# Kernel tuning notes

Measured on AMD Instinct MI355X. Metric: run time of the kernel, lower is better.

Reference implementation:

```python
import jax, jax.numpy as jnp
import numpy as np

EPS = 1e-6

def rms_norm(x):
    # RMSNorm over last dim, no learned weight (torch F.rms_norm without weight)
    return x * jax.lax.rsqrt(jnp.mean(jnp.square(x), axis=-1, keepdims=True) + EPS)

def apply_rotary_emb(x, cos, sin):
    # x: [b, t, h, d]; cos/sin: [t, d//2] -> broadcast [1, t, 1, d//2]
    half = x.shape[-1] // 2
    c = cos[None, :, None, :]
    s = sin[None, :, None, :]
    x1, x2 = x[..., :half], x[..., half:]
    return jnp.concatenate([x1 * c - x2 * s, x2 * c + x1 * s], axis=-1)

def setup_inputs() -> dict:
    key = jax.random.key(0)
    ks = jax.random.split(key, 16)
    B, T, E, H = 4, 2048, 1024, 16
    D = E // H
    inp = {
        "query": jax.random.normal(ks[0], (B, T, E), jnp.float32),
        "key": jax.random.normal(ks[1], (B, T, E), jnp.float32),
        "value": jax.random.normal(ks[2], (B, T, E), jnp.float32),
        "attn_mask": jnp.tril(jnp.ones((T, T), dtype=bool)),
        "cos": jnp.cos(jnp.arange(T)[:, None] / (10000.0 ** (jnp.arange(D // 2) / (D // 2)))[None, :]).astype(jnp.float32),
        "sin": jnp.sin(jnp.arange(T)[:, None] / (10000.0 ** (jnp.arange(D // 2) / (D // 2)))[None, :]).astype(jnp.float32),
        "Wq": jax.random.normal(ks[3], (E, E), jnp.float32) * 0.02,
        "bq": jnp.zeros((E,), jnp.float32),
        "Wk": jax.random.normal(ks[4], (E, E), jnp.float32) * 0.02,
        "bk": jnp.zeros((E,), jnp.float32),
        "Wv": jax.random.normal(ks[5], (E, E), jnp.float32) * 0.02,
        "bv": jnp.zeros((E,), jnp.float32),
        "Wo": jax.random.normal(ks[6], (E, E), jnp.float32) * 0.02,
        "bo": jnp.zeros((E,), jnp.float32),
    }
    return inp

def reference(query, key, value, attn_mask, cos, sin, Wq, bq, Wk, bk, Wv, bv, Wo, bo):
    B, T, E = query.shape
    H = 16
    D = E // H
    q = query @ Wq.T + bq
    k = key @ Wk.T + bk
    v = value @ Wv.T + bv
    q = q.reshape(B, T, H, D)
    k = k.reshape(B, T, H, D)
    v = v.reshape(B, T, H, D)
    q, k = rms_norm(q), rms_norm(k)
    q = apply_rotary_emb(q, cos, sin)
    k = apply_rotary_emb(k, cos, sin)
    # SDPA: [b, h, t, d] layout via einsum directly from [b, t, h, d]
    scale = 1.0 / jnp.sqrt(jnp.float32(D))
    scores = jnp.einsum('bqhd,bkhd->bhqk', q, k) * scale
    scores = jnp.where(attn_mask[None, None, :, :], scores, jnp.float32(-jnp.inf))
    attn = jax.nn.softmax(scores, axis=-1)
    o = jnp.einsum('bhqk,bkhd->bqhd', attn, v).reshape(B, T, E)
    return o @ Wo.T + bo
```

## Files before the change

kernel.cpp:

```cpp
#include <hip/hip_runtime.h>

typedef __bf16 bf16;
typedef __bf16 bf16x8 __attribute__((ext_vector_type(8)));
typedef __bf16 bf16x4 __attribute__((ext_vector_type(4)));
typedef float  floatx4 __attribute__((ext_vector_type(4)));

#define B_ 4
#define T_ 2048
#define E_ 1024
#define H_ 16
#define D_ 64
#define NTE_ (B_ * T_ * E_)

#define NEG_BIG (-1e30f)
#define SMAX2 12.2629081f

#define OFF_CQ 0ull
#define OFF_CK ((unsigned long long)NTE_)
#define OFF_CV (2ull * NTE_)
#define OFF_WQ (3ull * NTE_)
#define OFF_WK (OFF_WQ + 1048576ull)
#define OFF_WV (OFF_WK + 1048576ull)
#define OFF_WO (OFF_WV + 1048576ull)
__device__ bf16 g_conv[3ull * NTE_ + 4ull * 1048576ull];
__device__ bf16 g_scratch[5ull * NTE_];

__device__ __forceinline__ floatx4 mfma16(bf16x8 a, bf16x8 b, floatx4 c) {
  return __builtin_amdgcn_mfma_f32_16x16x32_bf16(a, b, c, 0, 0, 0);
}

__device__ __forceinline__ void async_copy16(void* lds, const void* g) {
  __builtin_amdgcn_global_load_lds(
      (const __attribute__((address_space(1))) unsigned int*)g,
      (__attribute__((address_space(3))) unsigned int*)lds, 16, 0, 0);
}

__global__ __launch_bounds__(256) void convert_all(const float4* __restrict__ q,
                                                   const float4* __restrict__ k,
                                                   const float4* __restrict__ v,
                                                   const float4* __restrict__ wq,
                                                   const float4* __restrict__ wk,
                                                   const float4* __restrict__ wv,
                                                   const float4* __restrict__ wo) {
  const float4* srcs[7] = {q, k, v, wq, wk, wv, wo};
  bf16x4* dsts[7] = {(bf16x4*)(g_conv + OFF_CQ), (bf16x4*)(g_conv + OFF_CK),
                     (bf16x4*)(g_conv + OFF_CV), (bf16x4*)(g_conv + OFF_WQ),
                     (bf16x4*)(g_conv + OFF_WK), (bf16x4*)(g_conv + OFF_WV),
                     (bf16x4*)(g_conv + OFF_WO)};
  const int n4s[7] = {NTE_ / 4, NTE_ / 4, NTE_ / 4, 262144, 262144, 262144, 262144};
  int i0 = blockIdx.x * 256 + threadIdx.x;
  int stride = gridDim.x * 256;
#pragma unroll
  for (int s = 0; s < 7; ++s) {
    const float4* sp = srcs[s];
    bf16x4* dp = dsts[s];
    int n4 = n4s[s];
    for (int i = i0; i < n4; i += stride) {
      float4 vv = sp[i];
      bf16x4 o;
      o[0] = (bf16)vv.x; o[1] = (bf16)vv.y; o[2] = (bf16)vv.z; o[3] = (bf16)vv.w;
      dp[i] = o;
    }
  }
}

__global__ __launch_bounds__(256) void gemm_qkv(const float* __restrict__ bq,
                                                const float* __restrict__ bk,
                                                const float* __restrict__ bv) {
  constexpr int K = 1024, N = 1024;
  const int z = blockIdx.z;
  const bf16* X = g_conv + OFF_CQ + (unsigned long long)z * NTE_;
  const bf16* W = g_conv + OFF_WQ + (unsigned long long)z * 1048576ull;
  const float* bias = (z == 0) ? bq : (z == 1) ? bk : bv;
  bf16* Y = g_scratch + (unsigned long long)z * NTE_;

  __shared__ bf16 sA[128 * 32];
  __shared__ bf16 sB[128 * 32];
  const int tid = threadIdx.x;
  const int w = tid >> 6;
  const int l = tid & 63;
  const int q = l >> 4;
  const int r = l & 15;
  const int M0 = blockIdx.x * 128;
  const int N0 = blockIdx.y * 128;
  const int wm = (w >> 1) * 64, wn = (w & 1) * 64;

  floatx4 acc[4][4];
  for (int mi = 0; mi < 4; ++mi)
    for (int ni = 0; ni < 4; ++ni) acc[mi][ni] = (floatx4){0.f, 0.f, 0.f, 0.f};

  for (int k0 = 0; k0 < K; k0 += 32) {
    __syncthreads();
#pragma unroll
    for (int i = 0; i < 2; ++i) {
      int idx = i * 256 + tid;
      int row = idx >> 2, cc = (idx & 3) << 3;
      bf16* dA = sA + (i * 2048 + w * 512);
      async_copy16(dA, X + (size_t)(M0 + row) * K + k0 + cc);
      bf16* dB = sB + (i * 2048 + w * 512);
      async_copy16(dB, W + (size_t)(N0 + row) * K + k0 + cc);
    }
    __syncthreads();

    bf16x8 a[4], b[4];
#pragma unroll
    for (int mi = 0; mi < 4; ++mi)
      a[mi] = *(const bf16x8*)(sA + (wm + mi * 16 + r) * 32 + q * 8);
#pragma unroll
    for (int ni = 0; ni < 4; ++ni)
      b[ni] = *(const bf16x8*)(sB + (wn + ni * 16 + r) * 32 + q * 8);
#pragma unroll
    for (int mi = 0; mi < 4; ++mi)
#pragma unroll
      for (int ni = 0; ni < 4; ++ni) acc[mi][ni] = mfma16(a[mi], b[ni], acc[mi][ni]);
  }

#pragma unroll
  for (int mi = 0; mi < 4; ++mi) {
    int rowbase = M0 + wm + mi * 16 + q * 4;
#pragma unroll
    for (int ni = 0; ni < 4; ++ni) {
      int col = N0 + wn + ni * 16 + r;
      float bv_ = bias[col];
#pragma unroll
      for (int rr = 0; rr < 4; ++rr) {
        Y[(size_t)(rowbase + rr) * N + col] = (bf16)(acc[mi][ni][rr] + bv_);
      }
    }
  }
}

__global__ __launch_bounds__(256) void gemm_out(const bf16* __restrict__ X,
                                                const bf16* __restrict__ W,
                                                const float* __restrict__ bias,
                                                float* __restrict__ Y) {
  constexpr int K = 1024, N = 1024;
  __shared__ bf16 sA[128 * 32];
  __shared__ bf16 sB[128 * 32];
  const int tid = threadIdx.x;
  const int w = tid >> 6;
  const int l = tid & 63;
  const int q = l >> 4;
  const int r = l & 15;
  const int M0 = blockIdx.x * 128;
  const int N0 = blockIdx.y * 128;
  const int wm = (w >> 1) * 64, wn = (w & 1) * 64;

  floatx4 acc[4][4];
  for (int mi = 0; mi < 4; ++mi)
    for (int ni = 0; ni < 4; ++ni) acc[mi][ni] = (floatx4){0.f, 0.f, 0.f, 0.f};

  for (int k0 = 0; k0 < K; k0 += 32) {
    __syncthreads();
#pragma unroll
    for (int i = 0; i < 2; ++i) {
      int idx = i * 256 + tid;
      int row = idx >> 2, cc = (idx & 3) << 3;
      bf16* dA = sA + (i * 2048 + w * 512);
      async_copy16(dA, X + (size_t)(M0 + row) * K + k0 + cc);
      bf16* dB = sB + (i * 2048 + w * 512);
      async_copy16(dB, W + (size_t)(N0 + row) * K + k0 + cc);
    }
    __syncthreads();

    bf16x8 a[4], b[4];
#pragma unroll
    for (int mi = 0; mi < 4; ++mi)
      a[mi] = *(const bf16x8*)(sA + (wm + mi * 16 + r) * 32 + q * 8);
#pragma unroll
    for (int ni = 0; ni < 4; ++ni)
      b[ni] = *(const bf16x8*)(sB + (wn + ni * 16 + r) * 32 + q * 8);
#pragma unroll
    for (int mi = 0; mi < 4; ++mi)
#pragma unroll
      for (int ni = 0; ni < 4; ++ni) acc[mi][ni] = mfma16(a[mi], b[ni], acc[mi][ni]);
  }

#pragma unroll
  for (int mi = 0; mi < 4; ++mi) {
    int rowbase = M0 + wm + mi * 16 + q * 4;
#pragma unroll
    for (int ni = 0; ni < 4; ++ni) {
      int col = N0 + wn + ni * 16 + r;
      float bv = bias[col];
#pragma unroll
      for (int rr = 0; rr < 4; ++rr) {
        Y[(size_t)(rowbase + rr) * N + col] = acc[mi][ni][rr] + bv;
      }
    }
  }
}

__global__ __launch_bounds__(256) void rmsnorm_rope(const float* __restrict__ cosb,
                                                    const float* __restrict__ sinb) {
  bf16* qp = g_scratch;
  bf16* kp = g_scratch + (unsigned long long)NTE_;
  constexpr int HR = B_ * T_ * H_;
  int gid = blockIdx.x * 16 + (threadIdx.x >> 4);
  int j = threadIdx.x & 15;
  bool isq = (gid < HR);
  bf16* base = isq ? qp : kp;
  float post = isq ? 0.18033688f : 1.0f;
  int row = gid & (HR - 1);
  int t = (row >> 4) & (T_ - 1);
  bf16* p = base + (size_t)row * 64 + j * 4;

  bf16x4 xv = *(const bf16x4*)p;
  float x[4], ss = 0.f;
#pragma unroll
  for (int i = 0; i < 4; ++i) { x[i] = (float)xv[i]; ss += x[i] * x[i]; }
#pragma unroll
  for (int m = 1; m < 16; m <<= 1) ss += __shfl_xor(ss, m, 64);
  float rs = rsqrtf(ss * (1.0f / 64.0f) + 1e-6f);

  float y[4], pr[4];
#pragma unroll
  for (int i = 0; i < 4; ++i) y[i] = x[i] * rs;
#pragma unroll
  for (int i = 0; i < 4; ++i) pr[i] = __shfl_xor(y[i], 8, 64);

  int dbase = (j & 7) * 4;
  bf16x4 ov;
#pragma unroll
  for (int i = 0; i < 4; ++i) {
    float c = cosb[t * 32 + dbase + i];
    float s = sinb[t * 32 + dbase + i];
    float o = (j < 8) ? (y[i] * c - pr[i] * s) : (y[i] * c + pr[i] * s);
    ov[i] = (bf16)(o * post);
  }
  *(bf16x4*)p = ov;
}

__global__ __launch_bounds__(256) void transpose_v() {
  const bf16* vp = g_scratch + 2ull * NTE_;
  bf16* vt = g_scratch + 3ull * NTE_;
  __shared__ bf16 tile[64][72];
  int bid = blockIdx.x;
  int tt = bid & 31;
  int bh = bid >> 5;
  int h = bh & 15, b = bh >> 4;
  int t0 = tt * 64;
  int tid = threadIdx.x;
#pragma unroll
  for (int i = 0; i < 2; ++i) {
    int idx = i * 256 + tid;
    int row = idx >> 3, cc = (idx & 7) * 8;
    bf16x8 v = *(const bf16x8*)(vp + (size_t)(b * T_ + t0 + row) * E_ + h * D_ + cc);
#pragma unroll
    for (int jj = 0; jj < 8; ++jj) tile[row][cc + jj] = v[jj];
  }
  __syncthreads();
#pragma unroll
  for (int i = 0; i < 2; ++i) {
    int idx = i * 256 + tid;
    int d = idx >> 3, tc = (idx & 7) * 8;
    bf16x8 v;
#pragma unroll
    for (int jj = 0; jj < 8; ++jj) v[jj] = tile[tc + jj][d];
    *(bf16x8*)(vt + ((size_t)bh * D_ + d) * T_ + t0 + tc) = v;
  }
}

#define KSTR 72
#define PSTR 72
__global__ __launch_bounds__(256, 4) void flash_attn() {
  const bf16* qp = g_scratch;
  const bf16* kp = g_scratch + (unsigned long long)NTE_;
  const bf16* vt = g_scratch + 3ull * NTE_;
  bf16* op = g_scratch + 4ull * NTE_;

  __shared__ __align__(16) bf16 sK[64 * KSTR];
  __shared__ __align__(16) bf16 sV[64 * KSTR];
  __shared__ __align__(16) bf16 sP[4 * 32 * PSTR];

  const int bid = blockIdx.x;
  const int xcd = bid & 7;
  const int lb = bid >> 3;
  const int bh = xcd * 8 + (lb & 7);
  const int qt = 15 - (lb >> 3);
  const int h = bh & 15, b = bh >> 4;
  const int tid = threadIdx.x, w = tid >> 6, l = tid & 63, g = l >> 4, r = l & 15;
  const int Q0 = qt * 128;
  const int qw = Q0 + w * 32;

  const bf16* kbase = kp + (size_t)(b * T_) * E_ + h * D_;
  const bf16* vbase = vt + (size_t)bh * D_ * T_;
  bf16* pw = sP + w * (32 * PSTR);

  bf16x8 ones;
#pragma unroll
  for (int i = 0; i < 8; ++i) ones[i] = (bf16)1.0f;

  bf16x8 qa[2][2];
#pragma unroll
  for (int qb = 0; qb < 2; ++qb)
#pragma unroll
    for (int hf = 0; hf < 2; ++hf)
      qa[qb][hf] = *(const bf16x8*)(qp + (size_t)(b * T_ + qw + qb * 16 + r) * E_ +
                                    h * D_ + hf * 32 + g * 8);

  floatx4 o_acc[2][4], l_acc[2];
#pragma unroll
  for (int qb = 0; qb < 2; ++qb) {
    l_acc[qb] = (floatx4){0.f, 0.f, 0.f, 0.f};
#pragma unroll
    for (int dt = 0; dt < 4; ++dt) o_acc[qb][dt] = (floatx4){0.f, 0.f, 0.f, 0.f};
  }

  int srow[2], scc[2];
#pragma unroll
  for (int i = 0; i < 2; ++i) {
    int idx = i * 256 + tid;
    srow[i] = idx >> 3;
    scc[i] = (idx & 7) * 8;
  }

  bf16x8 kreg[2], vreg[2];
#pragma unroll
  for (int i = 0; i < 2; ++i) {
    kreg[i] = *(const bf16x8*)(kbase + (size_t)srow[i] * E_ + scc[i]);
    vreg[i] = *(const bf16x8*)(vbase + (size_t)srow[i] * T_ + scc[i]);
  }

  const int lastKt = Q0 + 64;
  for (int kt0 = 0; kt0 <= lastKt; kt0 += 64) {
    __syncthreads();
#pragma unroll
    for (int i = 0; i < 2; ++i) {
      *(bf16x8*)(sK + srow[i] * KSTR + scc[i]) = kreg[i];
      *(bf16x8*)(sV + srow[i] * KSTR + scc[i]) = vreg[i];
    }
    if (kt0 < lastKt) {
      int kt1 = kt0 + 64;
#pragma unroll
      for (int i = 0; i < 2; ++i) {
        kreg[i] = *(const bf16x8*)(kbase + (size_t)(kt1 + srow[i]) * E_ + scc[i]);
        vreg[i] = *(const bf16x8*)(vbase + (size_t)srow[i] * T_ + kt1 + scc[i]);
      }
    }
    __syncthreads();

    if (kt0 <= qw + 31) {
      const bool needMask = (kt0 + 63 > qw);

#pragma unroll
      for (int sc = 0; sc < 4; ++sc) {
        bf16x8 kb0 = *(const bf16x8*)(sK + (sc * 16 + r) * KSTR + g * 8);
        bf16x8 kb1 = *(const bf16x8*)(sK + (sc * 16 + r) * KSTR + 32 + g * 8);
        floatx4 s0 = (floatx4){0.f, 0.f, 0.f, 0.f};
        floatx4 s1 = (floatx4){0.f, 0.f, 0.f, 0.f};
        s0 = mfma16(kb0, qa[0][0], s0);
        s0 = mfma16(kb1, qa[0][1], s0);
        s1 = mfma16(kb0, qa[1][0], s1);
        s1 = mfma16(kb1, qa[1][1], s1);

        if (needMask) {
          int kg = kt0 + sc * 16 + g * 4;
          int qg0 = qw + r;
          int qg1 = qw + 16 + r;
#pragma unroll
          for (int rr = 0; rr < 4; ++rr) {
            if (kg + rr > qg0) s0[rr] = NEG_BIG;
            if (kg + rr > qg1) s1[rr] = NEG_BIG;
          }
        }

        bf16x4 p0, p1;
#pragma unroll
        for (int rr = 0; rr < 4; ++rr) {
          p0[rr] = (bf16)exp2f(s0[rr] - SMAX2);
          p1[rr] = (bf16)exp2f(s1[rr] - SMAX2);
        }
        *(bf16x4*)(pw + r * PSTR + sc * 16 + g * 4) = p0;
        *(bf16x4*)(pw + (16 + r) * PSTR + sc * 16 + g * 4) = p1;
      }

#pragma unroll
      for (int kk = 0; kk < 2; ++kk) {
        bf16x8 vb[4];
#pragma unroll
        for (int dt = 0; dt < 4; ++dt)
          vb[dt] = *(const bf16x8*)(sV + (dt * 16 + r) * KSTR + kk * 32 + g * 8);
#pragma unroll
        for (int qb = 0; qb < 2; ++qb) {
          bf16x8 pa = *(const bf16x8*)(pw + (qb * 16 + r) * PSTR + kk * 32 + g * 8);
          l_acc[qb] = mfma16(pa, ones, l_acc[qb]);
#pragma unroll
          for (int dt = 0; dt < 4; ++dt)
            o_acc[qb][dt] = mfma16(pa, vb[dt], o_acc[qb][dt]);
        }
      }
    }
  }

  float linv[2][4];
#pragma unroll
  for (int qb = 0; qb < 2; ++qb)
#pragma unroll
    for (int rr = 0; rr < 4; ++rr) linv[qb][rr] = 1.0f / l_acc[qb][rr];
#pragma unroll
  for (int qb = 0; qb < 2; ++qb)
#pragma unroll
    for (int dt = 0; dt < 4; ++dt)
#pragma unroll
      for (int rr = 0; rr < 4; ++rr) {
        int t = qw + qb * 16 + g * 4 + rr;
        op[(size_t)(b * T_ + t) * E_ + h * D_ + dt * 16 + r] =
            (bf16)(o_acc[qb][dt][rr] * linv[qb][rr]);
      }
}

extern "C" void kernel_launch(void* const* d_in, const int* in_sizes, int n_in,
                              void* d_out, int out_size, void* d_ws, size_t ws_size,
                              hipStream_t stream) {
  float* out = (float*)d_out;

  void* cvp_ = nullptr;
  void* sp_ = nullptr;
  hipGetSymbolAddress(&cvp_, HIP_SYMBOL(g_conv));
  hipGetSymbolAddress(&sp_, HIP_SYMBOL(g_scratch));
  bf16* cv = (bf16*)cvp_;
  bf16* sc = (bf16*)sp_;

  const float* cosb = (const float*)d_in[4];
  const float* sinb = (const float*)d_in[5];
  const float* bq = (const float*)d_in[7];
  const float* bk = (const float*)d_in[9];
  const float* bv = (const float*)d_in[11];
  const float* bo = (const float*)d_in[13];

  convert_all<<<dim3(1024), dim3(256), 0, stream>>>(
      (const float4*)d_in[0], (const float4*)d_in[1], (const float4*)d_in[2],
      (const float4*)d_in[6], (const float4*)d_in[8], (const float4*)d_in[10],
      (const float4*)d_in[12]);

  bf16* op = sc + 4ull * NTE_;

  dim3 bb(256);
  gemm_qkv<<<dim3(64, 8, 3), bb, 0, stream>>>(bq, bk, bv);
  rmsnorm_rope<<<dim3(16384), bb, 0, stream>>>(cosb, sinb);
  transpose_v<<<dim3(2048), bb, 0, stream>>>();
  flash_attn<<<dim3(1024), bb, 0, stream>>>();
  gemm_out<<<dim3(64, 8), bb, 0, stream>>>(op, cv + OFF_WO, bo, out);
}
```

Baseline: 383.2 us.

## Rewrite QKV and output GEMMs with 256x256 tiles, double-buffered async loads, swizzled LDS

Replaces the 128x128, K=32 single-buffered GEMMs with a shared 256x256 tile core using 512 threads and K=64 steps. Global-to-LDS async copies are double-buffered with vmcnt waits, and the LDS layout is XOR-swizzled to avoid bank conflicts. MFMA blocks are interleaved with staged LDS reads under s_setprio, and block IDs are remapped for locality across XCDs. The aim is better data reuse and memory/compute overlap. In exchange it uses 128KB of shared memory, launches fewer blocks (384 and 128), and adds fragile hand-written barrier and waitcnt ordering.

Result: faster. 372.4 us (-2.8%).

```diff
diff --git a/kernel.cpp b/kernel.cpp
--- a/kernel.cpp
+++ b/kernel.cpp
@@ -64,131 +64,214 @@
   }
 }
 
-__global__ __launch_bounds__(256) void gemm_qkv(const float* __restrict__ bq,
-                                                const float* __restrict__ bk,
-                                                const float* __restrict__ bv) {
-  constexpr int K = 1024, N = 1024;
-  const int z = blockIdx.z;
-  const bf16* X = g_conv + OFF_CQ + (unsigned long long)z * NTE_;
-  const bf16* W = g_conv + OFF_WQ + (unsigned long long)z * 1048576ull;
-  const float* bias = (z == 0) ? bq : (z == 1) ? bk : bv;
-  bf16* Y = g_scratch + (unsigned long long)z * NTE_;
-
-  __shared__ bf16 sA[128 * 32];
-  __shared__ bf16 sB[128 * 32];
+template <bool OUTF32>
+__device__ __forceinline__ void gemm256_core(const bf16* __restrict__ X,
+                                             const bf16* __restrict__ W,
+                                             const float* __restrict__ bias,
+                                             void* __restrict__ Yv,
+                                             int M0, int N0) {
+  constexpr int NT = 16;
+  __shared__ __align__(16) char smem[131072];
+
   const int tid = threadIdx.x;
   const int w = tid >> 6;
   const int l = tid & 63;
   const int q = l >> 4;
   const int r = l & 15;
-  const int M0 = blockIdx.x * 128;
-  const int N0 = blockIdx.y * 128;
-  const int wm = (w >> 1) * 64, wn = (w & 1) * 64;
-
-  floatx4 acc[4][4];
-  for (int mi = 0; mi < 4; ++mi)
+  const int lrow = l >> 3;
+  const int qxr = q ^ (r & 7);
+  const int so0 = qxr << 4;
+  const int so1 = so0 ^ 64;
+  const int colb = ((l & 7) ^ lrow) << 4;
+
+  const int wm = (w >> 2) * 128;
+  const int wn = (w & 3) * 64;
+  const int halfA = w >> 2;
+  const int halfB = (w & 3) >> 1;
+
+  char* const sm = smem;
+  const char* const rdA = sm + halfA * 16384 + r * 128;
+  const char* const rdB = sm + 32768 + halfB * 16384 + ((w & 1) * 64 + r) * 128;
+  char* const stA = sm + w * 1024;
+  char* const stB = sm + 32768 + w * 1024;
+
+  const char* const gA = (const char*)X + ((size_t)(M0 + w * 8 + lrow)) * 2048 + colb;
+  const char* const gB = (const char*)W + ((size_t)(N0 + w * 8 + lrow)) * 2048 + colb;
+
+  floatx4 acc[8][4];
+#pragma unroll
+  for (int mi = 0; mi < 8; ++mi)
+#pragma unroll
     for (int ni = 0; ni < 4; ++ni) acc[mi][ni] = (floatx4){0.f, 0.f, 0.f, 0.f};
 
-  for (int k0 = 0; k0 < K; k0 += 32) {
-    __syncthreads();
-#pragma unroll
-    for (int i = 0; i < 2; ++i) {
-      int idx = i * 256 + tid;
-      int row = idx >> 2, cc = (idx & 3) << 3;
-      bf16* dA = sA + (i * 2048 + w * 512);
-      async_copy16(dA, X + (size_t)(M0 + row) * K + k0 + cc);
-      bf16* dB = sB + (i * 2048 + w * 512);
-      async_copy16(dB, W + (size_t)(N0 + row) * K + k0 + cc);
-    }
-    __syncthreads();
-
-    bf16x8 a[4], b[4];
+#define ST_A(p, h, t)                                          \
+  do {                                                         \
+    char* d_ = stA + (p) * 65536 + (h) * 16384;                \
+    const char* s_ = gA + (size_t)(h) * (128 * 2048) + (t) * 128; \
+    async_copy16(d_, s_);                                      \
+    async_copy16(d_ + 8192, s_ + 64 * 2048);                   \
+  } while (0)
+#define ST_B(p, h, t)                                          \
+  do {                                                         \
+    char* d_ = stB + (p) * 65536 + (h) * 16384;                \
+    const char* s_ = gB + (size_t)(h) * (128 * 2048) + (t) * 128; \
+    async_copy16(d_, s_);                                      \
+    async_copy16(d_ + 8192, s_ + 64 * 2048);                   \
+  } while (0)
+
+  ST_B(0, 0, 0); ST_B(0, 1, 0); ST_A(0, 0, 0); ST_A(0, 1, 0);
+  ST_B(1, 0, 1); ST_B(1, 1, 1); ST_A(1, 0, 1); ST_A(1, 1, 1);
+  asm volatile("s_waitcnt vmcnt(8)" ::: "memory");
+  __builtin_amdgcn_s_barrier();
+
+  bf16x8 aR[4][2], b0[2][2], b1[2][2];
+
+#pragma unroll 2
+  for (int t = 0; t < NT; ++t) {
+    const int p = t & 1;
+    const char* rA = rdA + p * 65536;
+    const char* rB = rdB + p * 65536;
+
+#pragma unroll
+    for (int mi = 0; mi < 4; ++mi) {
+      aR[mi][0] = *(const bf16x8*)(rA + mi * 2048 + so0);
+      aR[mi][1] = *(const bf16x8*)(rA + mi * 2048 + so1);
+    }
+#pragma unroll
+    for (int ni = 0; ni < 2; ++ni) {
+      b0[ni][0] = *(const bf16x8*)(rB + ni * 2048 + so0);
+      b0[ni][1] = *(const bf16x8*)(rB + ni * 2048 + so1);
+    }
+    __builtin_amdgcn_s_barrier();
+    asm volatile("s_waitcnt lgkmcnt(0)" ::: "memory");
+    __builtin_amdgcn_sched_barrier(0);
+    __builtin_amdgcn_s_setprio(1);
 #pragma unroll
     for (int mi = 0; mi < 4; ++mi)
-      a[mi] = *(const bf16x8*)(sA + (wm + mi * 16 + r) * 32 + q * 8);
-#pragma unroll
-    for (int ni = 0; ni < 4; ++ni)
-      b[ni] = *(const bf16x8*)(sB + (wn + ni * 16 + r) * 32 + q * 8);
+#pragma unroll
+      for (int ni = 0; ni < 2; ++ni) {
+        acc[mi][ni] = mfma16(aR[mi][0], b0[ni][0], acc[mi][ni]);
+        acc[mi][ni] = mfma16(aR[mi][1], b0[ni][1], acc[mi][ni]);
+      }
+    __builtin_amdgcn_s_setprio(0);
+    __builtin_amdgcn_s_barrier();
+
+#pragma unroll
+    for (int ni = 0; ni < 2; ++ni) {
+      b1[ni][0] = *(const bf16x8*)(rB + (ni + 2) * 2048 + so0);
+      b1[ni][1] = *(const bf16x8*)(rB + (ni + 2) * 2048 + so1);
+    }
+    __builtin_amdgcn_s_barrier();
+    asm volatile("s_waitcnt lgkmcnt(0)" ::: "memory");
+    __builtin_amdgcn_sched_barrier(0);
+    __builtin_amdgcn_s_setprio(1);
 #pragma unroll
     for (int mi = 0; mi < 4; ++mi)
 #pragma unroll
-      for (int ni = 0; ni < 4; ++ni) acc[mi][ni] = mfma16(a[mi], b[ni], acc[mi][ni]);
-  }
-
-#pragma unroll
-  for (int mi = 0; mi < 4; ++mi) {
-    int rowbase = M0 + wm + mi * 16 + q * 4;
-#pragma unroll
-    for (int ni = 0; ni < 4; ++ni) {
-      int col = N0 + wn + ni * 16 + r;
-      float bv_ = bias[col];
-#pragma unroll
-      for (int rr = 0; rr < 4; ++rr) {
-        Y[(size_t)(rowbase + rr) * N + col] = (bf16)(acc[mi][ni][rr] + bv_);
-      }
-    }
-  }
-}
-
-__global__ __launch_bounds__(256) void gemm_out(const bf16* __restrict__ X,
-                                                const bf16* __restrict__ W,
-                                                const float* __restrict__ bias,
-                                                float* __restrict__ Y) {
-  constexpr int K = 1024, N = 1024;
-  __shared__ bf16 sA[128 * 32];
-  __shared__ bf16 sB[128 * 32];
-  const int tid = threadIdx.x;
-  const int w = tid >> 6;
-  const int l = tid & 63;
-  const int q = l >> 4;
-  const int r = l & 15;
-  const int M0 = blockIdx.x * 128;
-  const int N0 = blockIdx.y * 128;
-  const int wm = (w >> 1) * 64, wn = (w & 1) * 64;
-
-  floatx4 acc[4][4];
-  for (int mi = 0; mi < 4; ++mi)
-    for (int ni = 0; ni < 4; ++ni) acc[mi][ni] = (floatx4){0.f, 0.f, 0.f, 0.f};
-
-  for (int k0 = 0; k0 < K; k0 += 32) {
-    __syncthreads();
-#pragma unroll
-    for (int i = 0; i < 2; ++i) {
-      int idx = i * 256 + tid;
-      int row = idx >> 2, cc = (idx & 3) << 3;
-      bf16* dA = sA + (i * 2048 + w * 512);
-      async_copy16(dA, X + (size_t)(M0 + row) * K + k0 + cc);
-      bf16* dB = sB + (i * 2048 + w * 512);
-      async_copy16(dB, W + (size_t)(N0 + row) * K + k0 + cc);
-    }
-    __syncthreads();
-
-    bf16x8 a[4], b[4];
+      for (int ni = 0; ni < 2; ++ni) {
+        acc[mi][ni + 2] = mfma16(aR[mi][0], b1[ni][0], acc[mi][ni + 2]);
+        acc[mi][ni + 2] = mfma16(aR[mi][1], b1[ni][1], acc[mi][ni + 2]);
+      }
+    __builtin_amdgcn_s_setprio(0);
+    __builtin_amdgcn_s_barrier();
+
+#pragma unroll
+    for (int mi = 0; mi < 4; ++mi) {
+      aR[mi][0] = *(const bf16x8*)(rA + 8192 + mi * 2048 + so0);
+      aR[mi][1] = *(const bf16x8*)(rA + 8192 + mi * 2048 + so1);
+    }
+    if (t + 2 < NT) { ST_B(p, 0, t + 2); ST_B(p, 1, t + 2); }
+    __builtin_amdgcn_s_barrier();
+    asm volatile("s_waitcnt lgkmcnt(0)" ::: "memory");
+    __builtin_amdgcn_sched_barrier(0);
+    __builtin_amdgcn_s_setprio(1);
 #pragma unroll
     for (int mi = 0; mi < 4; ++mi)
-      a[mi] = *(const bf16x8*)(sA + (wm + mi * 16 + r) * 32 + q * 8);
-#pragma unroll
-    for (int ni = 0; ni < 4; ++ni)
-      b[ni] = *(const bf16x8*)(sB + (wn + ni * 16 + r) * 32 + q * 8);
+#pragma unroll
+      for (int ni = 0; ni < 2; ++ni) {
+        acc[mi + 4][ni + 2] = mfma16(aR[mi][0], b1[ni][0], acc[mi + 4][ni + 2]);
+        acc[mi + 4][ni + 2] = mfma16(aR[mi][1], b1[ni][1], acc[mi + 4][ni + 2]);
+      }
+    __builtin_amdgcn_s_setprio(0);
+    __builtin_amdgcn_s_barrier();
+
+    if (t + 2 < NT) { ST_A(p, 0, t + 2); ST_A(p, 1, t + 2); }
+    __builtin_amdgcn_s_barrier();
+    __builtin_amdgcn_s_setprio(1);
 #pragma unroll
     for (int mi = 0; mi < 4; ++mi)
 #pragma unroll
-      for (int ni = 0; ni < 4; ++ni) acc[mi][ni] = mfma16(a[mi], b[ni], acc[mi][ni]);
-  }
-
-#pragma unroll
-  for (int mi = 0; mi < 4; ++mi) {
-    int rowbase = M0 + wm + mi * 16 + q * 4;
-#pragma unroll
-    for (int ni = 0; ni < 4; ++ni) {
-      int col = N0 + wn + ni * 16 + r;
-      float bv = bias[col];
-#pragma unroll
-      for (int rr = 0; rr < 4; ++rr) {
-        Y[(size_t)(rowbase + rr) * N + col] = acc[mi][ni][rr] + bv;
-      }
-    }
-  }
+      for (int ni = 0; ni < 2; ++ni) {
+        acc[mi + 4][ni] = mfma16(aR[mi][0], b0[ni][0], acc[mi + 4][ni]);
+        acc[mi + 4][ni] = mfma16(aR[mi][1], b0[ni][1], acc[mi + 4][ni]);
+      }
+    __builtin_amdgcn_s_setprio(0);
+    if (t + 2 < NT) {
+      asm volatile("s_waitcnt vmcnt(8)" ::: "memory");
+    } else {
+      asm volatile("s_waitcnt vmcnt(0)" ::: "memory");
+    }
+    __builtin_amdgcn_s_barrier();
+  }
+#undef ST_A
+#undef ST_B
+
+  float bvv[4];
+#pragma unroll
+  for (int ni = 0; ni < 4; ++ni) bvv[ni] = bias[N0 + wn + ni * 16 + r];
+
+  if (OUTF32) {
+    float* Y = (float*)Yv;
+#pragma unroll
+    for (int mi = 0; mi < 8; ++mi) {
+      int rowbase = M0 + wm + mi * 16 + q * 4;
+#pragma unroll
+      for (int ni = 0; ni < 4; ++ni) {
+        int col = N0 + wn + ni * 16 + r;
+#pragma unroll
+        for (int rr = 0; rr < 4; ++rr)
+          Y[(size_t)(rowbase + rr) * 1024 + col] = acc[mi][ni][rr] + bvv[ni];
+      }
+    }
+  } else {
+    bf16* Y = (bf16*)Yv;
+#pragma unroll
+    for (int mi = 0; mi < 8; ++mi) {
+      int rowbase = M0 + wm + mi * 16 + q * 4;
+#pragma unroll
+      for (int ni = 0; ni < 4; ++ni) {
+        int col = N0 + wn + ni * 16 + r;
+#pragma unroll
+        for (int rr = 0; rr < 4; ++rr)
+          Y[(size_t)(rowbase + rr) * 1024 + col] = (bf16)(acc[mi][ni][rr] + bvv[ni]);
+      }
+    }
+  }
+}
+
+__global__ __launch_bounds__(512, 2) void gemm_qkv(const float* __restrict__ bq,
+                                                   const float* __restrict__ bk,
+                                                   const float* __restrict__ bv) {
+  int bid = blockIdx.x;
+  int s = (bid & 7) * 48 + (bid >> 3);
+  int z = s >> 7;
+  int rm = s & 127;
+  int mt = rm >> 2, nt = rm & 3;
+  const bf16* X = g_conv + OFF_CQ + (unsigned long long)z * NTE_;
+  const bf16* W = g_conv + OFF_WQ + (unsigned long long)z * 1048576ull;
+  const float* bias = (z == 0) ? bq : (z == 1) ? bk : bv;
+  bf16* Y = g_scratch + (unsigned long long)z * NTE_;
+  gemm256_core<false>(X, W, bias, (void*)Y, mt * 256, nt * 256);
+}
+
+__global__ __launch_bounds__(512, 2) void gemm_out(const bf16* __restrict__ X,
+                                                   const bf16* __restrict__ W,
+                                                   const float* __restrict__ bias,
+                                                   float* __restrict__ Y) {
+  int bid = blockIdx.x;
+  int s = (bid & 7) * 16 + (bid >> 3);
+  int mt = s >> 2, nt = s & 3;
+  gemm256_core<true>(X, W, bias, (void*)Y, mt * 256, nt * 256);
 }
 
 __global__ __launch_bounds__(256) void rmsnorm_rope(const float* __restrict__ cosb,
@@ -436,10 +519,9 @@
 
   bf16* op = sc + 4ull * NTE_;
 
-  dim3 bb(256);
-  gemm_qkv<<<dim3(64, 8, 3), bb, 0, stream>>>(bq, bk, bv);
-  rmsnorm_rope<<<dim3(16384), bb, 0, stream>>>(cosb, sinb);
-  transpose_v<<<dim3(2048), bb, 0, stream>>>();
-  flash_attn<<<dim3(1024), bb, 0, stream>>>();
-  gemm_out<<<dim3(64, 8), bb, 0, stream>>>(op, cv + OFF_WO, bo, out);
-}
+  gemm_qkv<<<dim3(384), dim3(512), 0, stream>>>(bq, bk, bv);
+  rmsnorm_rope<<<dim3(16384), dim3(256), 0, stream>>>(cosb, sinb);
+  transpose_v<<<dim3(2048), dim3(256), 0, stream>>>();
+  flash_attn<<<dim3(1024), dim3(256), 0, stream>>>();
+  gemm_out<<<dim3(128), dim3(512), 0, stream>>>(op, cv + OFF_WO, bo, out);
+}
```
